# Performance work log

Measured on AMD Instinct MI355X. Metric: run time of the kernel, lower is better.

Reference implementation:

```python
import jax, jax.numpy as jnp
import numpy as np
from jax import lax

EPS_BN = 1e-5
EPS_AGG = 1e-6
N_NODES, READ_LEN, N_EDGES, DIM, KSZ, N_LAYERS = 20000, 64, 320000, 128, 20, 4


def batchnorm(x, g, b):
    # training-mode BatchNorm1d over the node/edge (batch) axis
    m = x.mean(0)
    v = x.var(0)
    return (x - m) * lax.rsqrt(v + EPS_BN) * g + b


def setup_inputs() -> dict:
    key = jax.random.key(0)
    ks = jax.random.split(key, 20)
    N, L, E, D, K, NL = N_NODES, READ_LEN, N_EDGES, DIM, KSZ, N_LAYERS
    rn = lambda k, shape, s=0.05: jax.random.normal(k, shape, dtype=jnp.float32) * s
    return dict(
        emb=rn(ks[0], (4, 3), 1.0),
        conv_w=rn(ks[1], (D, 3, K)), conv_b=jnp.zeros((D,), jnp.float32),
        ee_w=rn(ks[2], (D, 2)), ee_b=jnp.zeros((D,), jnp.float32),
        Aw=rn(ks[3], (NL, D, D)), Ab=jnp.zeros((NL, D), jnp.float32),
        Bw=rn(ks[4], (NL, D, D)), Bb=jnp.zeros((NL, D), jnp.float32),
        Cw=rn(ks[5], (NL, D, D)), Cb=jnp.zeros((NL, D), jnp.float32),
        Dw=rn(ks[6], (NL, D, D)), Db=jnp.zeros((NL, D), jnp.float32),
        Ew=rn(ks[7], (NL, D, D)), Eb=jnp.zeros((NL, D), jnp.float32),
        bnh_g=jnp.ones((NL, D), jnp.float32), bnh_b=jnp.zeros((NL, D), jnp.float32),
        bne_g=jnp.ones((NL, D), jnp.float32), bne_b=jnp.zeros((NL, D), jnp.float32),
        dec_w=rn(ks[8], (1, 3 * D)), dec_b=jnp.zeros((1,), jnp.float32),
        sim=jax.random.uniform(ks[9], (E,), dtype=jnp.float32),
        length=jax.random.uniform(ks[10], (E,), dtype=jnp.float32),
        reads=jax.random.randint(ks[11], (N, L), 0, 4, dtype=jnp.int32),
        src=jax.random.randint(ks[12], (E,), 0, N, dtype=jnp.int32),
        dst=jax.random.randint(ks[13], (E,), 0, N, dtype=jnp.int32),
    )


def reference(emb, conv_w, conv_b, ee_w, ee_b, Aw, Ab, Bw, Bb, Cw, Cb, Dw, Db,
              Ew, Eb, bnh_g, bnh_b, bne_g, bne_b, dec_w, dec_b,
              sim, length, reads, src, dst):
    n_nodes = reads.shape[0]
    # --- SequenceEncoder: base embedding -> Conv1d(valid) -> ReLU -> global max pool
    x = emb[reads]                                   # [N, L, 3]
    x = x.transpose(0, 2, 1)                          # [N, 3, L]
    x = lax.conv_general_dilated(x, conv_w, (1,), 'VALID',
                                 dimension_numbers=('NCH', 'OIH', 'NCH'))
    x = jax.nn.relu(x + conv_b[None, :, None])        # [N, D, L-K+1]
    h = x.max(axis=-1)                                # [N, D]
    # --- EdgeEncoder: Linear(2 -> D) on (overlap_similarity, overlap_length)
    e = jnp.stack([sim, length], axis=1) @ ee_w.T + ee_b   # [E, D]
    # --- GatedGCN stack
    for i in range(Aw.shape[0]):
        Ah = h @ Aw[i].T + Ab[i]
        Bh = h @ Bw[i].T + Bb[i]
        Dh = h @ Dw[i].T + Db[i]
        Eh = h @ Ew[i].T + Eb[i]
        Ce = e @ Cw[i].T + Cb[i]
        e_hat = Dh[dst] + Eh[src] + Ce                # [E, D] gather
        e = e + jax.nn.relu(batchnorm(e_hat, bne_g[i], bne_b[i]))
        sigma = jax.nn.sigmoid(e_hat)                 # edge gates
        num = jax.ops.segment_sum(sigma * Bh[src], dst, num_segments=n_nodes)
        den = jax.ops.segment_sum(sigma, dst, num_segments=n_nodes)
        h = h + jax.nn.relu(batchnorm(Ah + num / (den + EPS_AGG), bnh_g[i], bnh_b[i]))
    # --- EdgeDecoder: score each edge from (h_src, h_dst, e)
    z = jnp.concatenate([h[src], h[dst], e], axis=1)  # [E, 3D]
    return z @ dec_w.T + dec_b                        # [E, 1]
```

## Files before the change

### kernel.cpp

```cpp
#include <hip/hip_runtime.h>
#include <math.h>

#define NN 20000
#define LL 64
#define EE 320000
#define DD 128
#define KK 20
#define NLAYER 4
#define TOUT 45

#define EPS_BN 1e-5f
#define EPS_AGG 1e-6f

#define SEQ_KP 96
#define SEQ_AP 104

typedef unsigned short u16;
typedef __attribute__((ext_vector_type(8))) short short8;
typedef __attribute__((ext_vector_type(8))) _Float16 half8;
typedef __attribute__((ext_vector_type(4))) float floatx4;

__device__ __forceinline__ float b2f(u16 u) {
  union { unsigned int i; float f; } v;
  v.i = ((unsigned int)u) << 16;
  return v.f;
}
__device__ __forceinline__ u16 f2b(float f) {
  union { float f; unsigned int i; } v;
  v.f = f;
  unsigned int x = v.i;
  return (u16)((x + 0x7fffu + ((x >> 16) & 1u)) >> 16);
}

__global__ void zero_i32(int* __restrict__ p, int n)
{
  int i = blockIdx.x * 256 + threadIdx.x;
  if (i < n) p[i] = 0;
}

__global__ void diag_k(float* __restrict__ out, float v) { out[0] = v; }

__global__ void cast_weights(
    const float* __restrict__ Cw, const float* __restrict__ Aw,
    const float* __restrict__ Bw, const float* __restrict__ Dw,
    const float* __restrict__ Ew, u16* __restrict__ Cwb, u16* __restrict__ Anb,
    u16* __restrict__ Bnb, u16* __restrict__ Dnb, u16* __restrict__ Enb)
{
  int idx = blockIdx.x * 256 + threadIdx.x;
  int which = idx >> 16, off = idx & 65535;
  const float* s;
  u16* d;
  switch (which) {
    case 0: s = Cw; d = Cwb; break;
    case 1: s = Aw; d = Anb; break;
    case 2: s = Bw; d = Bnb; break;
    case 3: s = Dw; d = Dnb; break;
    default: s = Ew; d = Enb; break;
  }
  d[off] = f2b(s[off]);
}

__global__ void build_ws(const float* __restrict__ emb,
                         const float* __restrict__ conv_w,
                         _Float16* __restrict__ WSf)
{
  int idx = blockIdx.x * 256 + threadIdx.x;
  if (idx >= DD * SEQ_KP) return;
  int d = idx / SEQ_KP;
  int c = idx - d * SEQ_KP;
  float v = 0.f;
  if (c < 80) {
    int k = c >> 2, s = c & 3;
    v = emb[s * 3 + 0] * conv_w[d * 60 + k] +
        emb[s * 3 + 1] * conv_w[d * 60 + 20 + k] +
        emb[s * 3 + 2] * conv_w[d * 60 + 40 + k];
  }
  WSf[idx] = (_Float16)v;
}

__global__ __launch_bounds__(256) void seq_encoder(
    const _Float16* __restrict__ WSf, const float* __restrict__ conv_b,
    const int* __restrict__ reads, float* __restrict__ h,
    u16* __restrict__ h_bf)
{
  __shared__ int rd[LL];
  __shared__ _Float16 As[48][SEQ_AP];
  int tid = threadIdx.x;
  int n = blockIdx.x;
  if (tid < LL) rd[tid] = reads[n * LL + tid];
  __syncthreads();

#pragma unroll
  for (int it = 0; it < 20; it++) {
    int idx = tid + it * 256;
    if (idx < 48 * SEQ_AP) {
      int t = idx / SEQ_AP;
      int c = idx - t * SEQ_AP;
      _Float16 v = (_Float16)0.f;
      if (t < TOUT && c < 80) {
        int k = c >> 2, s = c & 3;
        v = (rd[t + k] == s) ? (_Float16)1.f : (_Float16)0.f;
      }
      (&As[0][0])[idx] = v;
    }
  }
  __syncthreads();

  int lane = tid & 63;
  int wv = tid >> 6;
  int m = lane & 15;
  int q = lane >> 4;

  half8 a[3][3];
#pragma unroll
  for (int mt = 0; mt < 3; mt++)
#pragma unroll
    for (int ks = 0; ks < 3; ks++)
      a[mt][ks] = *(const half8*)&As[mt * 16 + m][ks * 32 + q * 8];

  floatx4 acc[3][2];
#pragma unroll
  for (int mt = 0; mt < 3; mt++)
#pragma unroll
    for (int nt = 0; nt < 2; nt++) acc[mt][nt] = (floatx4){0.f, 0.f, 0.f, 0.f};

#pragma unroll
  for (int ks = 0; ks < 3; ks++) {
#pragma unroll
    for (int nt = 0; nt < 2; nt++) {
      int row = (wv * 2 + nt) * 16 + m;
      half8 b = *(const half8*)(WSf + (size_t)row * SEQ_KP + ks * 32 + q * 8);
#pragma unroll
      for (int mt = 0; mt < 3; mt++)
        acc[mt][nt] = __builtin_amdgcn_mfma_f32_16x16x32_f16(a[mt][ks], b,
                                                             acc[mt][nt], 0, 0, 0);
    }
  }

#pragma unroll
  for (int nt = 0; nt < 2; nt++) {
    float mx = -1e30f;
#pragma unroll
    for (int mt = 0; mt < 3; mt++) {
#pragma unroll
      for (int r = 0; r < 4; r++) {
        int row = mt * 16 + q * 4 + r;
        float v = acc[mt][nt][r];
        mx = (row < TOUT) ? fmaxf(mx, v) : mx;
      }
    }
    mx = fmaxf(mx, __shfl_xor(mx, 16, 64));
    mx = fmaxf(mx, __shfl_xor(mx, 32, 64));
    if (lane < 16) {
      int col = (wv * 2 + nt) * 16 + lane;
      float hv = fmaxf(mx + conv_b[col], 0.f);
      h[n * DD + col] = hv;
      h_bf[n * DD + col] = f2b(hv);
    }
  }
}

__global__ __launch_bounds__(256) void edge_encoder(
    const float* __restrict__ sim, const float* __restrict__ len,
    const float* __restrict__ ee_w, const float* __restrict__ ee_b,
    const int* __restrict__ ceid, u16* __restrict__ e)
{
  int idx = blockIdx.x * 256 + threadIdx.x;
  int c = idx & 127;
  int p = idx >> 7;
  int eid = ceid[p];
  float v = fmaf(sim[eid], ee_w[2 * c], fmaf(len[eid], ee_w[2 * c + 1], ee_b[c]));
  e[idx] = f2b(v);
}

__global__ void hist_kernel(const int* __restrict__ dst, int* __restrict__ deg)
{
  int i = blockIdx.x * 256 + threadIdx.x;
  if (i < EE) atomicAdd(&deg[dst[i]], 1);
}

__global__ __launch_bounds__(1024) void scan_kernel(
    const int* __restrict__ deg, int* __restrict__ off, int* __restrict__ cur)
{
  __shared__ int ss[1024];
  const int CH = 20;
  int tid = threadIdx.x;
  int base = tid * CH;
  int s = 0;
  for (int j = 0; j < CH; j++) {
    int i = base + j;
    if (i < NN) s += deg[i];
  }
  ss[tid] = s;
  __syncthreads();
  for (int o = 1; o < 1024; o <<= 1) {
    int v = (tid >= o) ? ss[tid - o] : 0;
    __syncthreads();
    ss[tid] += v;
    __syncthreads();
  }
  int run = (tid == 0) ? 0 : ss[tid - 1];
  for (int j = 0; j < CH; j++) {
    int i = base + j;
    if (i < NN) {
      off[i] = run;
      cur[i] = run;
      run += deg[i];
    }
  }
  if (base <= NN && NN < base + CH) off[NN] = run;
}

__global__ void scatter_kernel(const int* __restrict__ dst, int* __restrict__ cur,
                               int* __restrict__ csr)
{
  int i = blockIdx.x * 256 + threadIdx.x;
  if (i < EE) {
    int p = atomicAdd(&cur[dst[i]], 1);
    csr[p] = i;
  }
}

__global__ void build_perm(const int* __restrict__ ceid,
                           const int* __restrict__ src,
                           const int* __restrict__ dst,
                           int* __restrict__ sp, int* __restrict__ dp)
{
  int i = blockIdx.x * 256 + threadIdx.x;
  if (i < EE) {
    int eid = ceid[i];
    sp[i] = src[eid];
    dp[i] = dst[eid];
  }
}

__global__ __launch_bounds__(256) void gemm_node_mfma(
    const u16* __restrict__ hbf,
    const u16* __restrict__ W0, const u16* __restrict__ W1,
    const u16* __restrict__ W2, const u16* __restrict__ W3,
    const float* __restrict__ b0, const float* __restrict__ b1,
    const float* __restrict__ b2, const float* __restrict__ b3,
    u16* __restrict__ O0, u16* __restrict__ O1,
    u16* __restrict__ O2, u16* __restrict__ O3,
    float* __restrict__ stats)
{
  if (blockIdx.x == 0 && blockIdx.y == 0) {
    for (int j = threadIdx.x; j < 256 + 2 * 64 * DD; j += 256) stats[j] = 0.f;
  }
  const u16* W;
  const float* bias;
  u16* O;
  switch (blockIdx.y) {
    case 0: W = W0; bias = b0; O = O0; break;
    case 1: W = W1; bias = b1; O = O1; break;
    case 2: W = W2; bias = b2; O = O2; break;
    default: W = W3; bias = b3; O = O3; break;
  }
  int lane = threadIdx.x & 63;
  int wv = threadIdx.x >> 6;
  int rbase = blockIdx.x * 128 + wv * 32;
  int m = lane & 15;
  int q = lane >> 4;

  floatx4 acc[2][8];
#pragma unroll
  for (int rt = 0; rt < 2; rt++)
#pragma unroll
    for (int ct = 0; ct < 8; ct++) acc[rt][ct] = (floatx4){0.f, 0.f, 0.f, 0.f};

  int r0 = rbase + m;
  int r0c = r0 < NN ? r0 : NN - 1;
  int r1c = (r0 + 16) < NN ? (r0 + 16) : NN - 1;
  size_t a0base = (size_t)r0c * DD + q * 8;
  size_t a1base = (size_t)r1c * DD + q * 8;
  size_t bbase = (size_t)m * DD + q * 8;

#pragma unroll
  for (int ks = 0; ks < 4; ks++) {
    short8 a0 = *(const short8*)(hbf + a0base + ks * 32);
    short8 a1 = *(const short8*)(hbf + a1base + ks * 32);
#pragma unroll
    for (int ct = 0; ct < 8; ct++) {
      short8 b = *(const short8*)(W + bbase + (size_t)ct * 16 * DD + ks * 32);
      acc[0][ct] = __builtin_amdgcn_mfma_f32_16x16x32_bf16(a0, b, acc[0][ct], 0, 0, 0);
      acc[1][ct] = __builtin_amdgcn_mfma_f32_16x16x32_bf16(a1, b, acc[1][ct], 0, 0, 0);
    }
  }

  float cb[8];
#pragma unroll
  for (int ct = 0; ct < 8; ct++) cb[ct] = bias[ct * 16 + m];

#pragma unroll
  for (int rt = 0; rt < 2; rt++) {
#pragma unroll
    for (int r = 0; r < 4; r++) {
      int row = rbase + rt * 16 + q * 4 + r;
      if (row < NN) {
        u16* op = O + (size_t)row * DD + m;
#pragma unroll
        for (int ct = 0; ct < 8; ct++)
          op[ct * 16] = f2b(acc[rt][ct][r] + cb[ct]);
      }
    }
  }
}

__global__ __launch_bounds__(256) void gemm_edge_mfma(
    const u16* __restrict__ e, const u16* __restrict__ Cwb,
    const float* __restrict__ Cb, const u16* __restrict__ Dh,
    const u16* __restrict__ Eh, const int* __restrict__ sp,
    const int* __restrict__ dp, u16* __restrict__ ehat,
    float* __restrict__ p1e, float* __restrict__ p2e)
{
  __shared__ float s1s[4][128], s2s[4][128];
  int lane = threadIdx.x & 63;
  int wv = threadIdx.x >> 6;
  int rbase = blockIdx.x * 128 + wv * 32;
  int m = lane & 15;
  int q = lane >> 4;

  floatx4 acc[2][8];
#pragma unroll
  for (int rt = 0; rt < 2; rt++)
#pragma unroll
    for (int ct = 0; ct < 8; ct++) acc[rt][ct] = (floatx4){0.f, 0.f, 0.f, 0.f};

  size_t abase = (size_t)(rbase + m) * DD + q * 8;
  size_t bbase = (size_t)m * DD + q * 8;

#pragma unroll
  for (int ks = 0; ks < 4; ks++) {
    short8 a0 = *(const short8*)(e + abase + ks * 32);
    short8 a1 = *(const short8*)(e + abase + 16 * DD + ks * 32);
#pragma unroll
    for (int ct = 0; ct < 8; ct++) {
      short8 b = *(const short8*)(Cwb + bbase + (size_t)ct * 16 * DD + ks * 32);
      acc[0][ct] = __builtin_amdgcn_mfma_f32_16x16x32_bf16(a0, b, acc[0][ct], 0, 0, 0);
      acc[1][ct] = __builtin_amdgcn_mfma_f32_16x16x32_bf16(a1, b, acc[1][ct], 0, 0, 0);
    }
  }

  float cb[8], s1[8], s2[8];
#pragma unroll
  for (int ct = 0; ct < 8; ct++) {
    cb[ct] = Cb[ct * 16 + m];
    s1[ct] = 0.f;
    s2[ct] = 0.f;
  }

#pragma unroll
  for (int rt = 0; rt < 2; rt++) {
#pragma unroll
    for (int r = 0; r < 4; r++) {
      int row = rbase + rt * 16 + q * 4 + r;
      int dn = dp[row], sn = sp[row];
      const u16* dhp = Dh + (size_t)dn * DD + m;
      const u16* ehp = Eh + (size_t)sn * DD + m;
      u16* op = ehat + (size_t)row * DD + m;
#pragma unroll
      for (int ct = 0; ct < 8; ct++) {
        float v = acc[rt][ct][r] + cb[ct] + b2f(dhp[ct * 16]) + b2f(ehp[ct * 16]);
        op[ct * 16] = f2b(v);
        s1[ct] += v;
        s2[ct] = fmaf(v, v, s2[ct]);
      }
    }
  }

#pragma unroll
  for (int ct = 0; ct < 8; ct++) {
    float v1 = s1[ct], v2 = s2[ct];
    v1 += __shfl_down(v1, 16, 64);
    v1 += __shfl_down(v1, 32, 64);
    v2 += __shfl_down(v2, 16, 64);
    v2 += __shfl_down(v2, 32, 64);
    if (lane < 16) {
      s1s[wv][ct * 16 + lane] = v1;
      s2s[wv][ct * 16 + lane] = v2;
    }
  }
  __syncthreads();
  if (threadIdx.x < 128) {
    int c = threadIdx.x;
    atomicAdd(&p1e[c], s1s[0][c] + s1s[1][c] + s1s[2][c] + s1s[3][c]);
    atomicAdd(&p2e[c], s2s[0][c] + s2s[1][c] + s2s[2][c] + s2s[3][c]);
  }
}

__global__ __launch_bounds__(256) void agg_fused(
    const u16* __restrict__ ehat, u16* __restrict__ e,
    const u16* __restrict__ Bh, const u16* __restrict__ Ah,
    const float* __restrict__ p1e, const float* __restrict__ p2e,
    const float* __restrict__ bng, const float* __restrict__ bnb,
    const int* __restrict__ coff, const int* __restrict__ sp,
    float* __restrict__ xb, float* __restrict__ p1n, float* __restrict__ p2n)
{
  int n = blockIdx.x * 4 + (threadIdx.x >> 6);
  int lane = threadIdx.x & 63;
  int c2 = lane * 2;

  float2 P1 = *(const float2*)&p1e[c2];
  float2 P2 = *(const float2*)&p2e[c2];
  float2 gg = *(const float2*)&bng[c2];
  float2 bb = *(const float2*)&bnb[c2];
  const float inv = 1.f / (float)EE;
  float mean0 = P1.x * inv, mean1 = P1.y * inv;
  float var0 = fmaxf(P2.x * inv - mean0 * mean0, 0.f);
  float var1 = fmaxf(P2.y * inv - mean1 * mean1, 0.f);
  float sc0 = gg.x * rsqrtf(var0 + EPS_BN);
  float sc1 = gg.y * rsqrtf(var1 + EPS_BN);
  float sh0 = fmaf(-mean0, sc0, bb.x);
  float sh1 = fmaf(-mean1, sc1, bb.y);

  int b = coff[n], en = coff[n + 1];
  float n0 = 0.f, n1 = 0.f, d0 = 0.f, d1 = 0.f;
  for (int p = b; p < en; p++) {
    int sn = sp[p];
    ushort2 hv = *(const ushort2*)&ehat[(size_t)p * DD + c2];
    ushort2 ev = *(const ushort2*)&e[(size_t)p * DD + c2];
    float v0 = b2f(hv.x), v1 = b2f(hv.y);
    float eo0 = b2f(ev.x) + fmaxf(fmaf(v0, sc0, sh0), 0.f);
    float eo1 = b2f(ev.y) + fmaxf(fmaf(v1, sc1, sh1), 0.f);
    ushort2 w;
    w.x = f2b(eo0);
    w.y = f2b(eo1);
    *(ushort2*)&e[(size_t)p * DD + c2] = w;
    float s0 = 1.f / (1.f + __expf(-v0));
    float s1_ = 1.f / (1.f + __expf(-v1));
    d0 += s0;
    d1 += s1_;
    ushort2 bh = *(const ushort2*)&Bh[(size_t)sn * DD + c2];
    n0 = fmaf(s0, b2f(bh.x), n0);
    n1 = fmaf(s1_, b2f(bh.y), n1);
  }
  ushort2 av = *(const ushort2*)&Ah[(size_t)n * DD + c2];
  float x0 = b2f(av.x) + n0 / (d0 + EPS_AGG);
  float x1 = b2f(av.y) + n1 / (d1 + EPS_AGG);
  *(float2*)&xb[(size_t)n * DD + c2] = make_float2(x0, x1);
  float* pp1 = &p1n[(n & 63) * DD + c2];
  atomicAdd(pp1, x0);
  atomicAdd(pp1 + 1, x1);
  float* pp2 = &p2n[(n & 63) * DD + c2];
  atomicAdd(pp2, x0 * x0);
  atomicAdd(pp2 + 1, x1 * x1);
}

__global__ __launch_bounds__(256) void node_update(
    const float* __restrict__ x, const float* __restrict__ p1n,
    const float* __restrict__ p2n, const float* __restrict__ g,
    const float* __restrict__ b, float* __restrict__ h,
    u16* __restrict__ h_bf)
{
  int tid = threadIdx.x;
  int c = tid & 127;
  float s1 = 0.f, s2 = 0.f;
  for (int k = 0; k < 64; k++) {
    s1 += p1n[k * DD + c];
    s2 += p2n[k * DD + c];
  }
  const float inv = 1.f / (float)NN;
  float mean = s1 * inv;
  float var = fmaxf(s2 * inv - mean * mean, 0.f);
  float sc = g[c] * rsqrtf(var + EPS_BN);
  float sh = fmaf(-mean, sc, b[c]);
  for (int idx = blockIdx.x * 256 + tid; idx < NN * DD; idx += 256 * 256) {
    float hv = h[idx] + fmaxf(fmaf(x[idx], sc, sh), 0.f);
    h[idx] = hv;
    h_bf[idx] = f2b(hv);
  }
}

__global__ __launch_bounds__(256) void decoder_k(
    const float* __restrict__ h, const u16* __restrict__ e,
    const int* __restrict__ ceid, const int* __restrict__ sp,
    const int* __restrict__ dp, const float* __restrict__ dw,
    const float* __restrict__ db, float* __restrict__ out)
{
  int p = (blockIdx.x * 256 + threadIdx.x) >> 6;
  int lane = threadIdx.x & 63;
  int s = sp[p], dd = dp[p];
  float acc = 0.f;
#pragma unroll
  for (int half = 0; half < 2; half++) {
    int c = lane + half * 64;
    acc = fmaf(dw[c], h[(size_t)s * DD + c], acc);
    acc = fmaf(dw[DD + c], h[(size_t)dd * DD + c], acc);
    acc = fmaf(dw[2 * DD + c], b2f(e[(size_t)p * DD + c]), acc);
  }
#pragma unroll
  for (int o = 32; o > 0; o >>= 1) acc += __shfl_down(acc, o, 64);
  if (lane == 0) out[ceid[p]] = acc + db[0];
}

extern "C" void kernel_launch(void* const* d_in, const int* in_sizes, int n_in,
                              void* d_out, int out_size, void* d_ws, size_t ws_size,
                              hipStream_t stream)
{
  const float* emb = (const float*)d_in[0];
  const float* conv_w = (const float*)d_in[1];
  const float* conv_b = (const float*)d_in[2];
  const float* ee_w = (const float*)d_in[3];
  const float* ee_b = (const float*)d_in[4];
  const float* Aw = (const float*)d_in[5];
  const float* Ab = (const float*)d_in[6];
  const float* Bw = (const float*)d_in[7];
  const float* Bb = (const float*)d_in[8];
  const float* Cw = (const float*)d_in[9];
  const float* Cb = (const float*)d_in[10];
  const float* Dw = (const float*)d_in[11];
  const float* Db = (const float*)d_in[12];
  const float* Ew = (const float*)d_in[13];
  const float* Eb = (const float*)d_in[14];
  const float* bnh_g = (const float*)d_in[15];
  const float* bnh_b = (const float*)d_in[16];
  const float* bne_g = (const float*)d_in[17];
  const float* bne_b = (const float*)d_in[18];
  const float* dec_w = (const float*)d_in[19];
  const float* dec_b = (const float*)d_in[20];
  const float* sim = (const float*)d_in[21];
  const float* leng = (const float*)d_in[22];
  const int* reads = (const int*)d_in[23];
  const int* src = (const int*)d_in[24];
  const int* dst = (const int*)d_in[25];
  float* out = (float*)d_out;

  char* ws = (char*)d_ws;
  size_t off = 0;
  auto alloc = [&](size_t b) -> void* {
    void* p = ws + off;
    off += (b + 255) & ~(size_t)255;
    return p;
  };
  float* h = (float*)alloc((size_t)NN * DD * 4);
  u16* h_bf = (u16*)alloc((size_t)NN * DD * 2);
  u16* e = (u16*)alloc((size_t)EE * DD * 2);
  u16* ehat = (u16*)alloc((size_t)EE * DD * 2);
  u16* Ah = (u16*)alloc((size_t)NN * DD * 2);
  u16* Bh = (u16*)alloc((size_t)NN * DD * 2);
  u16* Dh = (u16*)alloc((size_t)NN * DD * 2);
  u16* Eh = (u16*)alloc((size_t)NN * DD * 2);
  float* xb = (float*)alloc((size_t)NN * DD * 4);
  float* stats = (float*)alloc((size_t)(256 + 2 * 64 * DD) * 4);
  float* p1e = stats;
  float* p2e = stats + 128;
  float* p1n = stats + 256;
  float* p2n = stats + 256 + 64 * DD;
  u16* Cwb = (u16*)alloc((size_t)NLAYER * DD * DD * 2);
  u16* Anb = (u16*)alloc((size_t)NLAYER * DD * DD * 2);
  u16* Bnb = (u16*)alloc((size_t)NLAYER * DD * DD * 2);
  u16* Dnb = (u16*)alloc((size_t)NLAYER * DD * DD * 2);
  u16* Enb = (u16*)alloc((size_t)NLAYER * DD * DD * 2);
  _Float16* WSf = (_Float16*)alloc((size_t)DD * SEQ_KP * 2);
  int* deg = (int*)alloc((size_t)NN * 4);
  int* coff = (int*)alloc((size_t)(NN + 1) * 4);
  int* ccur = (int*)alloc((size_t)NN * 4);
  int* ceid = (int*)alloc((size_t)EE * 4);
  int* sp = (int*)alloc((size_t)EE * 4);
  int* dp = (int*)alloc((size_t)EE * 4);

  if (off > ws_size) {
    diag_k<<<1, 1, 0, stream>>>(out, (float)ws_size);
    return;
  }

  zero_i32<<<(NN + 255) / 256, 256, 0, stream>>>(deg, NN);
  hist_kernel<<<(EE + 255) / 256, 256, 0, stream>>>(dst, deg);
  scan_kernel<<<1, 1024, 0, stream>>>(deg, coff, ccur);
  scatter_kernel<<<(EE + 255) / 256, 256, 0, stream>>>(dst, ccur, ceid);
  build_perm<<<(EE + 255) / 256, 256, 0, stream>>>(ceid, src, dst, sp, dp);

  cast_weights<<<5 * NLAYER * DD * DD / 256, 256, 0, stream>>>(
      Cw, Aw, Bw, Dw, Ew, Cwb, Anb, Bnb, Dnb, Enb);
  build_ws<<<(DD * SEQ_KP + 255) / 256, 256, 0, stream>>>(emb, conv_w, WSf);

  seq_encoder<<<NN, 256, 0, stream>>>(WSf, conv_b, reads, h, h_bf);
  edge_encoder<<<(EE * DD) / 256, 256, 0, stream>>>(sim, leng, ee_w, ee_b, ceid, e);

  for (int i = 0; i < NLAYER; i++) {
    size_t wo = (size_t)i * DD * DD;
    gemm_node_mfma<<<dim3((NN + 127) / 128, 4), 256, 0, stream>>>(
        h_bf, Anb + wo, Bnb + wo, Dnb + wo, Enb + wo,
        Ab + i * DD, Bb + i * DD, Db + i * DD, Eb + i * DD, Ah, Bh, Dh, Eh,
        stats);

    gemm_edge_mfma<<<EE / 128, 256, 0, stream>>>(e, Cwb + wo, Cb + i * DD, Dh,
                                                 Eh, sp, dp, ehat, p1e, p2e);

    agg_fused<<<NN / 4, 256, 0, stream>>>(ehat, e, Bh, Ah, p1e, p2e,
                                          bne_g + i * DD, bne_b + i * DD, coff,
                                          sp, xb, p1n, p2n);

    node_update<<<256, 256, 0, stream>>>(xb, p1n, p2n, bnh_g + i * DD,
                                         bnh_b + i * DD, h, h_bf);
  }

  decoder_k<<<EE / 4, 256, 0, stream>>>(h, e, ceid, sp, dp, dec_w, dec_b, out);
}
```

Measured before the change: 1.149 ms.

## Vectorize memory access with 16-byte loads/stores across edge and node kernels

Switches edge_encoder, the GEMM epilogues and agg_fused from 2-byte or 4-byte scattered accesses to 16-byte ushort8 vector accesses. The MFMA epilogues stage accumulator tiles through shared memory so each lane writes contiguous 8-column chunks, and the gathered Dh/Eh rows are read as vectors. agg_fused now processes 4 edges in parallel per wave with 8 channels per lane, then reduces across lane groups with shuffles. This aims to cut memory transaction count and raise bandwidth use, at the cost of extra LDS traffic, block-level barriers and per-lane register pressure.

```diff
diff --git a/kernel.cpp b/kernel.cpp
--- a/kernel.cpp
+++ b/kernel.cpp
@@ -17,6 +17,7 @@
 
 typedef unsigned short u16;
 typedef __attribute__((ext_vector_type(8))) short short8;
+typedef __attribute__((ext_vector_type(8))) unsigned short ushort8;
 typedef __attribute__((ext_vector_type(8))) _Float16 half8;
 typedef __attribute__((ext_vector_type(4))) float floatx4;
 
@@ -166,11 +167,17 @@
     const int* __restrict__ ceid, u16* __restrict__ e)
 {
   int idx = blockIdx.x * 256 + threadIdx.x;
-  int c = idx & 127;
-  int p = idx >> 7;
+  int p = idx >> 4;
+  int c0 = (idx & 15) * 8;
   int eid = ceid[p];
-  float v = fmaf(sim[eid], ee_w[2 * c], fmaf(len[eid], ee_w[2 * c + 1], ee_b[c]));
-  e[idx] = f2b(v);
+  float sv = sim[eid], lv = len[eid];
+  ushort8 o;
+#pragma unroll
+  for (int j = 0; j < 8; j++) {
+    int c = c0 + j;
+    o[j] = f2b(fmaf(sv, ee_w[2 * c], fmaf(lv, ee_w[2 * c + 1], ee_b[c])));
+  }
+  *(ushort8*)&e[(size_t)p * DD + c0] = o;
 }
 
 __global__ void hist_kernel(const int* __restrict__ dst, int* __restrict__ deg)
@@ -244,6 +251,7 @@
     u16* __restrict__ O2, u16* __restrict__ O3,
     float* __restrict__ stats)
 {
+  __shared__ float Gs[4][16][132];
   if (blockIdx.x == 0 && blockIdx.y == 0) {
     for (int j = threadIdx.x; j < 256 + 2 * 64 * DD; j += 256) stats[j] = 0.f;
   }
@@ -291,18 +299,27 @@
 #pragma unroll
   for (int ct = 0; ct < 8; ct++) cb[ct] = bias[ct * 16 + m];
 
+  int rg = lane >> 4, cg = lane & 15;
 #pragma unroll
   for (int rt = 0; rt < 2; rt++) {
 #pragma unroll
-    for (int r = 0; r < 4; r++) {
-      int row = rbase + rt * 16 + q * 4 + r;
-      if (row < NN) {
-        u16* op = O + (size_t)row * DD + m;
-#pragma unroll
-        for (int ct = 0; ct < 8; ct++)
-          op[ct * 16] = f2b(acc[rt][ct][r] + cb[ct]);
+    for (int ct = 0; ct < 8; ct++)
+#pragma unroll
+      for (int r = 0; r < 4; r++)
+        Gs[wv][q * 4 + r][ct * 16 + m] = acc[rt][ct][r] + cb[ct];
+    __syncthreads();
+#pragma unroll
+    for (int k = 0; k < 4; k++) {
+      int ri = k * 4 + rg;
+      int grow = rbase + rt * 16 + ri;
+      if (grow < NN) {
+        ushort8 ov;
+#pragma unroll
+        for (int j = 0; j < 8; j++) ov[j] = f2b(Gs[wv][ri][cg * 8 + j]);
+        *(ushort8*)(O + (size_t)grow * DD + cg * 8) = ov;
       }
     }
+    __syncthreads();
   }
 }
 
@@ -313,6 +330,7 @@
     const int* __restrict__ dp, u16* __restrict__ ehat,
     float* __restrict__ p1e, float* __restrict__ p2e)
 {
+  __shared__ float Gs[4][16][132];
   __shared__ float s1s[4][128], s2s[4][128];
   int lane = threadIdx.x & 63;
   int wv = threadIdx.x >> 6;
@@ -341,43 +359,54 @@
     }
   }
 
-  float cb[8], s1[8], s2[8];
-#pragma unroll
-  for (int ct = 0; ct < 8; ct++) {
-    cb[ct] = Cb[ct * 16 + m];
-    s1[ct] = 0.f;
-    s2[ct] = 0.f;
-  }
+  float cb[8];
+#pragma unroll
+  for (int ct = 0; ct < 8; ct++) cb[ct] = Cb[ct * 16 + m];
+
+  int rg = lane >> 4, cg = lane & 15;
+  int c0 = cg * 8;
+  float s1[8], s2[8];
+#pragma unroll
+  for (int j = 0; j < 8; j++) { s1[j] = 0.f; s2[j] = 0.f; }
 
 #pragma unroll
   for (int rt = 0; rt < 2; rt++) {
 #pragma unroll
-    for (int r = 0; r < 4; r++) {
-      int row = rbase + rt * 16 + q * 4 + r;
-      int dn = dp[row], sn = sp[row];
-      const u16* dhp = Dh + (size_t)dn * DD + m;
-      const u16* ehp = Eh + (size_t)sn * DD + m;
-      u16* op = ehat + (size_t)row * DD + m;
-#pragma unroll
-      for (int ct = 0; ct < 8; ct++) {
-        float v = acc[rt][ct][r] + cb[ct] + b2f(dhp[ct * 16]) + b2f(ehp[ct * 16]);
-        op[ct * 16] = f2b(v);
-        s1[ct] += v;
-        s2[ct] = fmaf(v, v, s2[ct]);
+    for (int ct = 0; ct < 8; ct++)
+#pragma unroll
+      for (int r = 0; r < 4; r++)
+        Gs[wv][q * 4 + r][ct * 16 + m] = acc[rt][ct][r] + cb[ct];
+    __syncthreads();
+#pragma unroll
+    for (int k = 0; k < 4; k++) {
+      int ri = k * 4 + rg;
+      int grow = rbase + rt * 16 + ri;
+      int dn = dp[grow], sn = sp[grow];
+      ushort8 dh = *(const ushort8*)(Dh + (size_t)dn * DD + c0);
+      ushort8 eh = *(const ushort8*)(Eh + (size_t)sn * DD + c0);
+      ushort8 ov;
+#pragma unroll
+      for (int j = 0; j < 8; j++) {
+        float v = Gs[wv][ri][c0 + j] + b2f(dh[j]) + b2f(eh[j]);
+        ov[j] = f2b(v);
+        s1[j] += v;
+        s2[j] = fmaf(v, v, s2[j]);
       }
-    }
-  }
-
-#pragma unroll
-  for (int ct = 0; ct < 8; ct++) {
-    float v1 = s1[ct], v2 = s2[ct];
-    v1 += __shfl_down(v1, 16, 64);
-    v1 += __shfl_down(v1, 32, 64);
-    v2 += __shfl_down(v2, 16, 64);
-    v2 += __shfl_down(v2, 32, 64);
-    if (lane < 16) {
-      s1s[wv][ct * 16 + lane] = v1;
-      s2s[wv][ct * 16 + lane] = v2;
+      *(ushort8*)(ehat + (size_t)grow * DD + c0) = ov;
+    }
+    __syncthreads();
+  }
+
+#pragma unroll
+  for (int j = 0; j < 8; j++) {
+    float a1 = s1[j], a2 = s2[j];
+    a1 += __shfl_down(a1, 16, 64);
+    a1 += __shfl_down(a1, 32, 64);
+    a2 += __shfl_down(a2, 16, 64);
+    a2 += __shfl_down(a2, 32, 64);
+    if (rg == 0) {
+      s1s[wv][c0 + j] = a1;
+      s2s[wv][c0 + j] = a2;
     }
   }
   __syncthreads();
@@ -396,54 +425,74 @@
     const int* __restrict__ coff, const int* __restrict__ sp,
     float* __restrict__ xb, float* __restrict__ p1n, float* __restrict__ p2n)
 {
-  int n = blockIdx.x * 4 + (threadIdx.x >> 6);
+  int wv = threadIdx.x >> 6;
+  int n = blockIdx.x * 4 + wv;
   int lane = threadIdx.x & 63;
-  int c2 = lane * 2;
-
-  float2 P1 = *(const float2*)&p1e[c2];
-  float2 P2 = *(const float2*)&p2e[c2];
-  float2 gg = *(const float2*)&bng[c2];
-  float2 bb = *(const float2*)&bnb[c2];
+  int rg = lane >> 4, cg = lane & 15;
+  int c0 = cg * 8;
+
+  float sc[8], sh[8];
   const float inv = 1.f / (float)EE;
-  float mean0 = P1.x * inv, mean1 = P1.y * inv;
-  float var0 = fmaxf(P2.x * inv - mean0 * mean0, 0.f);
-  float var1 = fmaxf(P2.y * inv - mean1 * mean1, 0.f);
-  float sc0 = gg.x * rsqrtf(var0 + EPS_BN);
-  float sc1 = gg.y * rsqrtf(var1 + EPS_BN);
-  float sh0 = fmaf(-mean0, sc0, bb.x);
-  float sh1 = fmaf(-mean1, sc1, bb.y);
+#pragma unroll
+  for (int j = 0; j < 8; j++) {
+    int c = c0 + j;
+    float mean = p1e[c] * inv;
+    float var = fmaxf(p2e[c] * inv - mean * mean, 0.f);
+    sc[j] = bng[c] * rsqrtf(var + EPS_BN);
+    sh[j] = fmaf(-mean, sc[j], bnb[c]);
+  }
 
   int b = coff[n], en = coff[n + 1];
-  float n0 = 0.f, n1 = 0.f, d0 = 0.f, d1 = 0.f;
-  for (int p = b; p < en; p++) {
-    int sn = sp[p];
-    ushort2 hv = *(const ushort2*)&ehat[(size_t)p * DD + c2];
-    ushort2 ev = *(const ushort2*)&e[(size_t)p * DD + c2];
-    float v0 = b2f(hv.x), v1 = b2f(hv.y);
-    float eo0 = b2f(ev.x) + fmaxf(fmaf(v0, sc0, sh0), 0.f);
-    float eo1 = b2f(ev.y) + fmaxf(fmaf(v1, sc1, sh1), 0.f);
-    ushort2 w;
-    w.x = f2b(eo0);
-    w.y = f2b(eo1);
-    *(ushort2*)&e[(size_t)p * DD + c2] = w;
-    float s0 = 1.f / (1.f + __expf(-v0));
-    float s1_ = 1.f / (1.f + __expf(-v1));
-    d0 += s0;
-    d1 += s1_;
-    ushort2 bh = *(const ushort2*)&Bh[(size_t)sn * DD + c2];
-    n0 = fmaf(s0, b2f(bh.x), n0);
-    n1 = fmaf(s1_, b2f(bh.y), n1);
-  }
-  ushort2 av = *(const ushort2*)&Ah[(size_t)n * DD + c2];
-  float x0 = b2f(av.x) + n0 / (d0 + EPS_AGG);
-  float x1 = b2f(av.y) + n1 / (d1 + EPS_AGG);
-  *(float2*)&xb[(size_t)n * DD + c2] = make_float2(x0, x1);
-  float* pp1 = &p1n[(n & 63) * DD + c2];
-  atomicAdd(pp1, x0);
-  atomicAdd(pp1 + 1, x1);
-  float* pp2 = &p2n[(n & 63) * DD + c2];
-  atomicAdd(pp2, x0 * x0);
-  atomicAdd(pp2 + 1, x1 * x1);
+  float num[8], den[8];
+#pragma unroll
+  for (int j = 0; j < 8; j++) { num[j] = 0.f; den[j] = 0.f; }
+
+  for (int pb = b; pb < en; pb += 4) {
+    int p = pb + rg;
+    if (p < en) {
+      int sn = sp[p];
+      ushort8 hv = *(const ushort8*)&ehat[(size_t)p * DD + c0];
+      ushort8 ev = *(const ushort8*)&e[(size_t)p * DD + c0];
+      ushort8 bh = *(const ushort8*)&Bh[(size_t)sn * DD + c0];
+      ushort8 eo;
+#pragma unroll
+      for (int j = 0; j < 8; j++) {
+        float v = b2f(hv[j]);
+        eo[j] = f2b(b2f(ev[j]) + fmaxf(fmaf(v, sc[j], sh[j]), 0.f));
+        float s = 1.f / (1.f + __expf(-v));
+        den[j] += s;
+        num[j] = fmaf(s, b2f(bh[j]), num[j]);
+      }
+      *(ushort8*)&e[(size_t)p * DD + c0] = eo;
+    }
+  }
+
+#pragma unroll
+  for (int j = 0; j < 8; j++) {
+    num[j] += __shfl_down(num[j], 16, 64);
+    num[j] += __shfl_down(num[j], 32, 64);
+    den[j] += __shfl_down(den[j], 16, 64);
+    den[j] += __shfl_down(den[j], 32, 64);
+  }
+
+  if (rg == 0) {
+    ushort8 av = *(const ushort8*)&Ah[(size_t)n * DD + c0];
+    float x[8];
+#pragma unroll
+    for (int j = 0; j < 8; j++)
+      x[j] = b2f(av[j]) + num[j] / (den[j] + EPS_AGG);
+    float4 xa = make_float4(x[0], x[1], x[2], x[3]);
+    float4 xbv = make_float4(x[4], x[5], x[6], x[7]);
+    *(float4*)&xb[(size_t)n * DD + c0] = xa;
+    *(float4*)&xb[(size_t)n * DD + c0 + 4] = xbv;
+    float* pp1 = &p1n[(n & 63) * DD + c0];
+    float* pp2 = &p2n[(n & 63) * DD + c0];
+#pragma unroll
+    for (int j = 0; j < 8; j++) {
+      atomicAdd(pp1 + j, x[j]);
+      atomicAdd(pp2 + j, x[j] * x[j]);
+    }
+  }
 }
 
 __global__ __launch_bounds__(256) void node_update(
@@ -575,7 +624,8 @@
   build_ws<<<(DD * SEQ_KP + 255) / 256, 256, 0, stream>>>(emb, conv_w, WSf);
 
   seq_encoder<<<NN, 256, 0, stream>>>(WSf, conv_b, reads, h, h_bf);
-  edge_encoder<<<(EE * DD) / 256, 256, 0, stream>>>(sim, leng, ee_w, ee_b, ceid, e);
+  edge_encoder<<<(EE * DD / 8) / 256, 256, 0, stream>>>(sim, leng, ee_w, ee_b,
+                                                        ceid, e);
 
   for (int i = 0; i < NLAYER; i++) {
     size_t wo = (size_t)i * DD * DD;
```

Result: slower. 1.698 ms (+47.7%).
